# Kernel optimization log

Measured on AMD Instinct MI355X. Metric: run time of the kernel, lower is better.

Reference implementation:

```python
import jax, jax.numpy as jnp
import numpy as np

NUM_HEADS = 8
EMBED_CH = 512   # k channels
OUT_CH = 256     # v channels
MASK_CURRENT = False
NEG_INF = -1e30


def setup_inputs() -> dict:
    key = jax.random.key(0)
    ks = jax.random.split(key, 7)
    N, C, H, W = 8, 256, 32, 32
    s = lambda fan: 1.0 / np.sqrt(fan)
    return {
        "x": jax.random.normal(ks[0], (N, C, H, W), jnp.float32),
        "Wq": jax.random.normal(ks[1], (EMBED_CH, C), jnp.float32) * s(C),
        "bq": jax.random.normal(ks[2], (EMBED_CH,), jnp.float32) * 0.01,
        "Wkv": jax.random.normal(ks[3], (EMBED_CH + OUT_CH, C), jnp.float32) * s(C),
        "bkv": jax.random.normal(ks[4], (EMBED_CH + OUT_CH,), jnp.float32) * 0.01,
        "Wo": jax.random.normal(ks[5], (OUT_CH, OUT_CH), jnp.float32) * s(OUT_CH),
        "bo": jax.random.normal(ks[6], (OUT_CH,), jnp.float32) * 0.01,
    }


def _to_multihead(t, n, T):
    # t: [n, h*d, T] with channel layout '(h d)' -> [n, h, T, d]
    h = NUM_HEADS
    return t.reshape(n, h, -1, T).transpose(0, 1, 3, 2)


def reference(x, Wq, bq, Wkv, bkv, Wo, bo):
    n, C, H, W = x.shape
    T = H * W
    xf = x.reshape(n, C, T)  # flatten spatial dims into sequence

    # 1x1 convs == pointwise channel GEMMs
    q = jnp.einsum('oc,nct->not', Wq, xf) + bq[None, :, None]
    kv = jnp.einsum('oc,nct->not', Wkv, xf) + bkv[None, :, None]
    k, v = kv[:, :EMBED_CH], kv[:, EMBED_CH:]

    q = _to_multihead(q, n, T)   # [n, h, T, dk]
    k = _to_multihead(k, n, T)   # [n, h, T, dk]
    v = _to_multihead(v, n, T)   # [n, h, T, dv]

    dk = k.shape[-1]
    scale = 1.0 / np.sqrt(dk).astype(np.float32)

    # causal mask over flattened spatial positions (lower-triangular)
    diag = -1 if MASK_CURRENT else 0
    mask = jnp.tril(jnp.ones((T, T), dtype=bool), k=diag)  # [T, T]

    attn = jnp.einsum('nhtd,nhsd->nhts', q, k) * scale
    attn = jnp.where(mask[None, None], attn, NEG_INF)
    attn = jax.nn.softmax(attn, axis=-1)
    attn = jnp.where(mask[None, None], attn, 0.0)

    out = jnp.einsum('nhts,nhsd->nhtd', attn, v)            # [n, h, T, dv]
    out = out.transpose(0, 1, 3, 2).reshape(n, OUT_CH, T)   # n (h d) t

    out = jnp.einsum('oc,nct->not', Wo, out) + bo[None, :, None]
    return out.reshape(n, OUT_CH, H, W)
```

## Files before the change

### kernel.cpp

```cpp
#include <hip/hip_runtime.h>
#include <hip/hip_bf16.h>
#include <math.h>

typedef __bf16 bf16;
typedef __attribute__((ext_vector_type(4))) __bf16 bf16x4;
typedef __attribute__((ext_vector_type(8))) __bf16 bf16x8;
typedef __attribute__((ext_vector_type(4))) float f32x4;

#define T_DIM 1024
#define C_DIM 256
#define HEADS 8

static __device__ __forceinline__ int tb(int row, int col) {
  return row * 128 + ((((col >> 3) ^ row) & 7) << 4) + ((col & 7) << 1);
}

static __device__ __forceinline__ void gl16(const char* g, char* l) {
  __builtin_amdgcn_global_load_lds(
      (const __attribute__((address_space(1))) unsigned int*)g,
      (__attribute__((address_space(3))) unsigned int*)l, 16, 0, 0);
}
static __device__ __forceinline__ void stage16k(const char* g, char* l, int tid) {
  const int w = (tid >> 6) * 1024, ln = (tid & 63) * 16;
#pragma unroll
  for (int i = 0; i < 4; ++i) gl16(g + i * 4096 + w + ln, l + i * 4096 + w);
}
static __device__ __forceinline__ void stage8k(const char* g, char* l, int tid) {
  const int w = (tid >> 6) * 1024, ln = (tid & 63) * 16;
#pragma unroll
  for (int i = 0; i < 2; ++i) gl16(g + i * 4096 + w + ln, l + i * 4096 + w);
}
static __device__ __forceinline__ void stage4k(const char* g, char* l, int tid) {
  gl16(g + (tid >> 6) * 1024 + (tid & 63) * 16, l + (tid >> 6) * 1024);
}

__global__ __launch_bounds__(256) void k_prep(const float* __restrict__ x,
    const float* __restrict__ Wq, const float* __restrict__ Wkv, const float* __restrict__ Wo,
    char* __restrict__ xTt, char* __restrict__ Wbt, char* __restrict__ Wot) {
  const int tid = threadIdx.x;
  const int b = blockIdx.x;
  if (b < 512) {
    __shared__ float tile[64][65];
    const int n = b >> 6, rem = b & 63, tt64 = rem >> 2, ct = (rem & 3) << 6;
    const float* xp = x + ((size_t)n * C_DIM + ct) * T_DIM + tt64 * 64;
    const int t = tid & 63, c0 = tid >> 6;
#pragma unroll
    for (int i = 0; i < 16; ++i) tile[c0 + i * 4][t] = xp[(size_t)(c0 + i * 4) * T_DIM + t];
    __syncthreads();
    char* dst = xTt + (((size_t)(n * 8 + (tt64 >> 1))) * 4 + (rem & 3)) * 16384;
    const int rbase = (tt64 & 1) * 64;
#pragma unroll
    for (int i = 0; i < 2; ++i) {
      const int idx = tid + i * 256;
      const int tl = idx >> 3, c8 = (idx & 7) * 8;
      bf16x8 v;
#pragma unroll
      for (int j = 0; j < 8; ++j) v[j] = (bf16)tile[c8 + j][tl];
      *(bf16x8*)(dst + tb(rbase + tl, c8)) = v;
    }
  } else {
    const bool isWo = (b >= 532);
    const int o0 = (b - (isWo ? 532 : 512)) * 64;
#pragma unroll
    for (int i = 0; i < 8; ++i) {
      const int idx = tid + i * 256;
      const int row = idx >> 5, c8 = (idx & 31) * 8;
      const int o = o0 + row;
      const float* src = isWo ? (Wo + (size_t)o * C_DIM + c8)
                              : (o < 512 ? Wq + (size_t)o * C_DIM + c8
                                         : Wkv + (size_t)(o - 512) * C_DIM + c8);
      float4 a = *(const float4*)src;
      float4 bq4 = *(const float4*)(src + 4);
      bf16x8 v;
      v[0]=(bf16)a.x; v[1]=(bf16)a.y; v[2]=(bf16)a.z; v[3]=(bf16)a.w;
      v[4]=(bf16)bq4.x; v[5]=(bf16)bq4.y; v[6]=(bf16)bq4.z; v[7]=(bf16)bq4.w;
      char* base = isWo ? Wot : Wbt;
      char* dst = base + (((size_t)(o >> 7)) * 4 + (c8 >> 6)) * 16384;
      *(bf16x8*)(dst + tb(o & 127, c8 & 63)) = v;
    }
  }
}

__global__ __launch_bounds__(256) void k_qkv(const char* __restrict__ Wbt, const char* __restrict__ xTt,
    const float* __restrict__ bq, const float* __restrict__ bkv,
    bf16* __restrict__ q_ws, char* __restrict__ Kt, char* __restrict__ Vt) {
  __shared__ __attribute__((aligned(128))) unsigned char smem[32768];
  const int tid = threadIdx.x;
  const int nt = blockIdx.x, mt = blockIdx.y, n = blockIdx.z;
  const int w = tid >> 6, lane = tid & 63, lrow = lane & 15, lg = lane >> 4;
  const int wm = (w >> 1) * 64, wn = (w & 1) * 64;
  const char* gA = Wbt + (size_t)mt * 65536;
  const char* gB = xTt + ((size_t)(n * 8 + nt)) * 65536;

  f32x4 acc[4][4] = {};
#pragma unroll 1
  for (int kk = 0; kk < 4; ++kk) {
    stage16k(gA + kk * 16384, (char*)smem, tid);
    stage16k(gB + kk * 16384, (char*)smem + 16384, tid);
    __syncthreads();
    const char* As = (const char*)smem;
    const char* Bs = As + 16384;
    bf16x8 af[4][2], bv[4][2];
#pragma unroll
    for (int mi = 0; mi < 4; ++mi)
#pragma unroll
      for (int kh = 0; kh < 2; ++kh)
        af[mi][kh] = *(const bf16x8*)(As + tb(wm + mi * 16 + lrow, kh * 32 + lg * 8));
#pragma unroll
    for (int ni = 0; ni < 4; ++ni)
#pragma unroll
      for (int kh = 0; kh < 2; ++kh)
        bv[ni][kh] = *(const bf16x8*)(Bs + tb(wn + ni * 16 + lrow, kh * 32 + lg * 8));
#pragma unroll
    for (int kh = 0; kh < 2; ++kh)
#pragma unroll
      for (int mi = 0; mi < 4; ++mi)
#pragma unroll
        for (int ni = 0; ni < 4; ++ni)
          acc[mi][ni] = __builtin_amdgcn_mfma_f32_16x16x32_bf16(af[mi][kh], bv[ni][kh], acc[mi][ni], 0, 0, 0);
    __syncthreads();
  }

  const int obase = mt * 128 + wm + lg * 4;
  const int tcol0 = nt * 128 + wn + lrow;
#pragma unroll
  for (int mi = 0; mi < 4; ++mi) {
    const int o = obase + mi * 16;
    if (mt < 4) {
      const float4 bb = *(const float4*)(bq + o);
      const int nh = n * 8 + (o >> 6), d = o & 63;
      bf16* qrow = q_ws + (size_t)nh * (T_DIM * 64) + d;
#pragma unroll
      for (int ni = 0; ni < 4; ++ni) {
        const int t = tcol0 + ni * 16;
        f32x4 v = acc[mi][ni];
        bf16x4 pk;
        pk[0]=(bf16)(v[0]+bb.x); pk[1]=(bf16)(v[1]+bb.y); pk[2]=(bf16)(v[2]+bb.z); pk[3]=(bf16)(v[3]+bb.w);
        *(bf16x4*)(qrow + (size_t)t * 64) = pk;
      }
    } else if (mt < 8) {
      const int o2 = o - 512;
      const float4 bb = *(const float4*)(bkv + o2);
      const int nh = n * 8 + (o2 >> 6), d = o2 & 63;
      char* tbase = Kt + (size_t)nh * 16 * 8192;
#pragma unroll
      for (int ni = 0; ni < 4; ++ni) {
        const int t = tcol0 + ni * 16;
        f32x4 v = acc[mi][ni];
        bf16x4 pk;
        pk[0]=(bf16)(v[0]+bb.x); pk[1]=(bf16)(v[1]+bb.y); pk[2]=(bf16)(v[2]+bb.z); pk[3]=(bf16)(v[3]+bb.w);
        *(bf16x4*)(tbase + (t >> 6) * 8192 + tb(t & 63, d)) = pk;
      }
    } else {
      const int o3 = o - 1024;
      const float4 bb = *(const float4*)(bkv + 512 + o3);
      const float* bbp = (const float*)&bb;
      const int nh = n * 8 + (o3 >> 5), dv = o3 & 31;
      char* tbase = Vt + (size_t)nh * 16 * 4096;
#pragma unroll
      for (int ni = 0; ni < 4; ++ni) {
        const int t = tcol0 + ni * 16;
        f32x4 v = acc[mi][ni];
        char* tile = tbase + (t >> 6) * 4096;
#pragma unroll
        for (int r = 0; r < 4; ++r)
          *(bf16*)(tile + tb(dv + r, t & 63)) = (bf16)(v[r] + bbp[r]);
      }
    }
  }
}

__global__ __launch_bounds__(256) void k_attn(const bf16* __restrict__ q_ws,
    const char* __restrict__ Kt, const char* __restrict__ Vt, char* __restrict__ attTt) {
  __shared__ __attribute__((aligned(128))) unsigned char smem[20480];
  const int tid = threadIdx.x;
  const int nh = blockIdx.x, qp = blockIdx.y;
  const int w = tid >> 6, lane = tid & 63, lrow = lane & 15, lg = lane >> 4;

  const char* Ktb = Kt + (size_t)nh * 16 * 8192;
  const char* Vtb = Vt + (size_t)nh * 16 * 4096;
  const char* Kb = (const char*)smem;
  const char* Vb = (const char*)smem + 8192;
  char* pw = (char*)smem + 12288 + w * 2048;
  const int n = nh >> 3, h = nh & 7;
  const float s2 = 0.18033688f;

#pragma unroll 1
  for (int ph = 0; ph < 2; ++ph) {
    const int qt = ph ? (15 - qp) : qp;
    const int tg = qt * 64 + w * 16 + lrow;
    const bf16* qbase = q_ws + ((size_t)nh * T_DIM + tg) * 64;
    const bf16x8 qf0 = *(const bf16x8*)(qbase + lg * 8);
    const bf16x8 qf1 = *(const bf16x8*)(qbase + 32 + lg * 8);

    float m = -INFINITY, l = 0.f;
    f32x4 oacc[2] = {};

    for (int st = 0; st <= qt; ++st) {
      stage8k(Ktb + st * 8192, (char*)smem, tid);
      stage4k(Vtb + st * 4096, (char*)smem + 8192, tid);
      __syncthreads();

      f32x4 sacc[4];
#pragma unroll
      for (int rt = 0; rt < 4; ++rt) {
        f32x4 a = {0.f, 0.f, 0.f, 0.f};
        bf16x8 kf0 = *(const bf16x8*)(Kb + tb(rt * 16 + lrow, lg * 8));
        a = __builtin_amdgcn_mfma_f32_16x16x32_bf16(kf0, qf0, a, 0, 0, 0);
        bf16x8 kf1 = *(const bf16x8*)(Kb + tb(rt * 16 + lrow, 32 + lg * 8));
        a = __builtin_amdgcn_mfma_f32_16x16x32_bf16(kf1, qf1, a, 0, 0, 0);
        sacc[rt] = a;
      }

      float p[16];
      const bool diag = (st == qt);
      const int tl = w * 16 + lrow;
#pragma unroll
      for (int rt = 0; rt < 4; ++rt)
#pragma unroll
        for (int r = 0; r < 4; ++r) {
          float v = sacc[rt][r] * s2;
          if (diag && (rt * 16 + lg * 4 + r) > tl) v = -INFINITY;
          p[rt * 4 + r] = v;
        }

      float pmax = p[0];
#pragma unroll
      for (int i = 1; i < 16; ++i) pmax = fmaxf(pmax, p[i]);
      pmax = fmaxf(pmax, __shfl_xor(pmax, 16));
      pmax = fmaxf(pmax, __shfl_xor(pmax, 32));
      const float mn = fmaxf(m, pmax);
      const float corr = exp2f(m - mn);
      float ps = 0.f;
#pragma unroll
      for (int i = 0; i < 16; ++i) { p[i] = exp2f(p[i] - mn); ps += p[i]; }
      ps += __shfl_xor(ps, 16);
      ps += __shfl_xor(ps, 32);
      l = l * corr + ps;
      m = mn;
      oacc[0] = oacc[0] * corr;
      oacc[1] = oacc[1] * corr;

#pragma unroll
      for (int rt = 0; rt < 4; ++rt) {
        bf16x4 pk;
#pragma unroll
        for (int r = 0; r < 4; ++r) pk[r] = (bf16)p[rt * 4 + r];
        *(bf16x4*)(pw + tb(lrow, rt * 16 + lg * 4)) = pk;
      }

#pragma unroll
      for (int ks = 0; ks < 2; ++ks) {
        bf16x8 pf = *(const bf16x8*)(pw + tb(lrow, ks * 32 + lg * 8));
#pragma unroll
        for (int dt = 0; dt < 2; ++dt) {
          bf16x8 vf = *(const bf16x8*)(Vb + tb(dt * 16 + lrow, ks * 32 + lg * 8));
          oacc[dt] = __builtin_amdgcn_mfma_f32_16x16x32_bf16(vf, pf, oacc[dt], 0, 0, 0);
        }
      }
      __syncthreads();
    }

    const float inv = 1.0f / l;
    const int ntt = tg >> 7, row = tg & 127;
#pragma unroll
    for (int dt = 0; dt < 2; ++dt) {
      const int c = h * 32 + dt * 16 + lg * 4;
      char* tile = attTt + (((size_t)(n * 8 + ntt)) * 4 + (c >> 6)) * 16384;
      bf16x4 pk;
#pragma unroll
      for (int r = 0; r < 4; ++r) pk[r] = (bf16)(oacc[dt][r] * inv);
      *(bf16x4*)(tile + tb(row, c & 63)) = pk;
    }
  }
}

__global__ __launch_bounds__(256) void k_proj(const char* __restrict__ attTt,
    const char* __restrict__ Wot, const float* __restrict__ bo, float* __restrict__ out) {
  __shared__ __attribute__((aligned(128))) unsigned char smem[24576];
  const int tid = threadIdx.x;
  const int tm = blockIdx.x, om = blockIdx.y, n = blockIdx.z;
  const int w = tid >> 6, lane = tid & 63, lrow = lane & 15, lg = lane >> 4;
  const int wm = (w >> 1) * 64, wn = (w & 1) * 32;
  const char* gA = attTt + ((size_t)(n * 8 + tm)) * 65536;
  const char* gB = Wot + (size_t)(om >> 1) * 65536 + (om & 1) * 8192;

  f32x4 acc[4][2] = {};
#pragma unroll 1
  for (int kk = 0; kk < 4; ++kk) {
    stage16k(gA + kk * 16384, (char*)smem, tid);
    stage8k(gB + kk * 16384, (char*)smem + 16384, tid);
    __syncthreads();
    const char* As = (const char*)smem;
    const char* Bs = As + 16384;
    bf16x8 af[4][2], bv[2][2];
#pragma unroll
    for (int mi = 0; mi < 4; ++mi)
#pragma unroll
      for (int kh = 0; kh < 2; ++kh)
        af[mi][kh] = *(const bf16x8*)(As + tb(wm + mi * 16 + lrow, kh * 32 + lg * 8));
#pragma unroll
    for (int ni = 0; ni < 2; ++ni)
#pragma unroll
      for (int kh = 0; kh < 2; ++kh)
        bv[ni][kh] = *(const bf16x8*)(Bs + tb(wn + ni * 16 + lrow, kh * 32 + lg * 8));
#pragma unroll
    for (int kh = 0; kh < 2; ++kh)
#pragma unroll
      for (int mi = 0; mi < 4; ++mi)
#pragma unroll
        for (int ni = 0; ni < 2; ++ni)
          acc[mi][ni] = __builtin_amdgcn_mfma_f32_16x16x32_bf16(af[mi][kh], bv[ni][kh], acc[mi][ni], 0, 0, 0);
    __syncthreads();
  }

  const int t0b = tm * 128 + wm + lg * 4;
  const int ob = om * 64 + wn + lrow;
#pragma unroll
  for (int mi = 0; mi < 4; ++mi) {
    const int t0 = t0b + mi * 16;
#pragma unroll
    for (int ni = 0; ni < 2; ++ni) {
      const int o = ob + ni * 16;
      const float bb = bo[o];
      f32x4 v = acc[mi][ni];
      v[0] += bb; v[1] += bb; v[2] += bb; v[3] += bb;
      *(f32x4*)(out + ((size_t)(n * C_DIM + o)) * T_DIM + t0) = v;
    }
  }
}

extern "C" void kernel_launch(void* const* d_in, const int* in_sizes, int n_in,
                              void* d_out, int out_size, void* d_ws, size_t ws_size,
                              hipStream_t stream) {
  const float* x   = (const float*)d_in[0];
  const float* Wq  = (const float*)d_in[1];
  const float* bq  = (const float*)d_in[2];
  const float* Wkv = (const float*)d_in[3];
  const float* bkv = (const float*)d_in[4];
  const float* Wo  = (const float*)d_in[5];
  const float* bo  = (const float*)d_in[6];
  float* out = (float*)d_out;

  char* ws = (char*)d_ws;
  char* xTt   = ws;
  char* Wbt   = ws + (4u  << 20);
  char* Wot   = ws + (5u  << 20);
  bf16* q_ws  = (bf16*)(ws + (6u << 20));
  char* Kt    = ws + (14u << 20);
  char* Vt    = ws + (22u << 20);
  char* attTt = ws + (26u << 20);

  k_prep<<<536, 256, 0, stream>>>(x, Wq, Wkv, Wo, xTt, Wbt, Wot);
  k_qkv<<<dim3(8, 10, 8), 256, 0, stream>>>(Wbt, xTt, bq, bkv, q_ws, Kt, Vt);
  k_attn<<<dim3(64, 8), 256, 0, stream>>>(q_ws, Kt, Vt, attTt);
  k_proj<<<dim3(8, 4, 8), 256, 0, stream>>>(attTt, Wot, bo, out);
}
```

Baseline: 60.59 us.

## Share K/V tiles across paired query tiles, stage V via LDS, vectorize prep

The attention kernel now handles both paired query tiles (qp and 15-qp) in one pass over the key/value tiles. It stages two K/V tiles per barrier and reuses each staged tile for both query tiles, which halves global K/V loads and barriers, and it adds s_setprio around the MFMA sections. The QKV kernel writes V through a padded LDS transpose so the global stores are vectorized 16-byte writes instead of scattered 2-byte ones. The x transpose in prep uses float4 loads, and the output projection uses smaller 64-row tiles to double the grid. In exchange the attention kernel doubles its LDS use and keeps two sets of accumulators live.

```diff
diff --git a/kernel.cpp b/kernel.cpp
--- a/kernel.cpp
+++ b/kernel.cpp
@@ -43,9 +43,13 @@
     __shared__ float tile[64][65];
     const int n = b >> 6, rem = b & 63, tt64 = rem >> 2, ct = (rem & 3) << 6;
     const float* xp = x + ((size_t)n * C_DIM + ct) * T_DIM + tt64 * 64;
-    const int t = tid & 63, c0 = tid >> 6;
-#pragma unroll
-    for (int i = 0; i < 16; ++i) tile[c0 + i * 4][t] = xp[(size_t)(c0 + i * 4) * T_DIM + t];
+    const int t4 = (tid & 15) * 4, c0 = tid >> 4;
+#pragma unroll
+    for (int i = 0; i < 4; ++i) {
+      const int c = c0 + i * 16;
+      float4 v = *(const float4*)(xp + (size_t)c * T_DIM + t4);
+      tile[c][t4] = v.x; tile[c][t4 + 1] = v.y; tile[c][t4 + 2] = v.z; tile[c][t4 + 3] = v.w;
+    }
     __syncthreads();
     char* dst = xTt + (((size_t)(n * 8 + (tt64 >> 1))) * 4 + (rem & 3)) * 16384;
     const int rbase = (tt64 & 1) * 64;
@@ -84,7 +88,7 @@
 __global__ __launch_bounds__(256) void k_qkv(const char* __restrict__ Wbt, const char* __restrict__ xTt,
     const float* __restrict__ bq, const float* __restrict__ bkv,
     bf16* __restrict__ q_ws, char* __restrict__ Kt, char* __restrict__ Vt) {
-  __shared__ __attribute__((aligned(128))) unsigned char smem[32768];
+  __shared__ __attribute__((aligned(128))) unsigned char smem[34816];
   const int tid = threadIdx.x;
   const int nt = blockIdx.x, mt = blockIdx.y, n = blockIdx.z;
   const int w = tid >> 6, lane = tid & 63, lrow = lane & 15, lg = lane >> 4;
@@ -123,179 +127,215 @@
 
   const int obase = mt * 128 + wm + lg * 4;
   const int tcol0 = nt * 128 + wn + lrow;
-#pragma unroll
-  for (int mi = 0; mi < 4; ++mi) {
-    const int o = obase + mi * 16;
-    if (mt < 4) {
-      const float4 bb = *(const float4*)(bq + o);
-      const int nh = n * 8 + (o >> 6), d = o & 63;
-      bf16* qrow = q_ws + (size_t)nh * (T_DIM * 64) + d;
+  if (mt < 8) {
+#pragma unroll
+    for (int mi = 0; mi < 4; ++mi) {
+      const int o = obase + mi * 16;
+      if (mt < 4) {
+        const float4 bb = *(const float4*)(bq + o);
+        const int nh = n * 8 + (o >> 6), d = o & 63;
+        bf16* qrow = q_ws + (size_t)nh * (T_DIM * 64) + d;
+#pragma unroll
+        for (int ni = 0; ni < 4; ++ni) {
+          const int t = tcol0 + ni * 16;
+          f32x4 v = acc[mi][ni];
+          bf16x4 pk;
+          pk[0]=(bf16)(v[0]+bb.x); pk[1]=(bf16)(v[1]+bb.y); pk[2]=(bf16)(v[2]+bb.z); pk[3]=(bf16)(v[3]+bb.w);
+          *(bf16x4*)(qrow + (size_t)t * 64) = pk;
+        }
+      } else {
+        const int o2 = o - 512;
+        const float4 bb = *(const float4*)(bkv + o2);
+        const int nh = n * 8 + (o2 >> 6), d = o2 & 63;
+        char* tbase = Kt + (size_t)nh * 16 * 8192;
+#pragma unroll
+        for (int ni = 0; ni < 4; ++ni) {
+          const int t = tcol0 + ni * 16;
+          f32x4 v = acc[mi][ni];
+          bf16x4 pk;
+          pk[0]=(bf16)(v[0]+bb.x); pk[1]=(bf16)(v[1]+bb.y); pk[2]=(bf16)(v[2]+bb.z); pk[3]=(bf16)(v[3]+bb.w);
+          *(bf16x4*)(tbase + (t >> 6) * 8192 + tb(t & 63, d)) = pk;
+        }
+      }
+    }
+  } else {
+    bf16* tp = (bf16*)smem;
+#pragma unroll
+    for (int mi = 0; mi < 4; ++mi) {
+      const int o3g = (mt - 8) * 128 + wm + mi * 16 + lg * 4;
+      const float4 bb = *(const float4*)(bkv + 512 + o3g);
+      const float* bbp = (const float*)&bb;
+      const int o3l = wm + mi * 16 + lg * 4;
 #pragma unroll
       for (int ni = 0; ni < 4; ++ni) {
-        const int t = tcol0 + ni * 16;
+        const int tl = wn + ni * 16 + lrow;
         f32x4 v = acc[mi][ni];
-        bf16x4 pk;
-        pk[0]=(bf16)(v[0]+bb.x); pk[1]=(bf16)(v[1]+bb.y); pk[2]=(bf16)(v[2]+bb.z); pk[3]=(bf16)(v[3]+bb.w);
-        *(bf16x4*)(qrow + (size_t)t * 64) = pk;
+#pragma unroll
+        for (int r = 0; r < 4; ++r)
+          tp[(o3l + r) * 132 + tl] = (bf16)(v[r] + bbp[r]);
       }
-    } else if (mt < 8) {
-      const int o2 = o - 512;
-      const float4 bb = *(const float4*)(bkv + o2);
-      const int nh = n * 8 + (o2 >> 6), d = o2 & 63;
-      char* tbase = Kt + (size_t)nh * 16 * 8192;
-#pragma unroll
-      for (int ni = 0; ni < 4; ++ni) {
-        const int t = tcol0 + ni * 16;
-        f32x4 v = acc[mi][ni];
-        bf16x4 pk;
-        pk[0]=(bf16)(v[0]+bb.x); pk[1]=(bf16)(v[1]+bb.y); pk[2]=(bf16)(v[2]+bb.z); pk[3]=(bf16)(v[3]+bb.w);
-        *(bf16x4*)(tbase + (t >> 6) * 8192 + tb(t & 63, d)) = pk;
-      }
-    } else {
-      const int o3 = o - 1024;
-      const float4 bb = *(const float4*)(bkv + 512 + o3);
-      const float* bbp = (const float*)&bb;
-      const int nh = n * 8 + (o3 >> 5), dv = o3 & 31;
-      char* tbase = Vt + (size_t)nh * 16 * 4096;
-#pragma unroll
-      for (int ni = 0; ni < 4; ++ni) {
-        const int t = tcol0 + ni * 16;
-        f32x4 v = acc[mi][ni];
-        char* tile = tbase + (t >> 6) * 4096;
-#pragma unroll
-        for (int r = 0; r < 4; ++r)
-          *(bf16*)(tile + tb(dv + r, t & 63)) = (bf16)(v[r] + bbp[r]);
-      }
+    }
+    __syncthreads();
+    const int row = tid >> 1, half = tid & 1;
+    const int o3 = (mt - 8) * 128 + row;
+    const int nh = n * 8 + (o3 >> 5), dv = o3 & 31;
+    char* tile = Vt + (size_t)nh * 16 * 4096 + (nt * 2 + half) * 4096;
+    const bf16* src = tp + row * 132 + half * 64;
+#pragma unroll
+    for (int g = 0; g < 8; ++g) {
+      bf16x4 lo = *(const bf16x4*)(src + g * 8);
+      bf16x4 hi = *(const bf16x4*)(src + g * 8 + 4);
+      bf16x8 vv;
+      vv[0]=lo[0]; vv[1]=lo[1]; vv[2]=lo[2]; vv[3]=lo[3];
+      vv[4]=hi[0]; vv[5]=hi[1]; vv[6]=hi[2]; vv[7]=hi[3];
+      *(bf16x8*)(tile + tb(dv, g * 8)) = vv;
     }
   }
 }
 
 __global__ __launch_bounds__(256) void k_attn(const bf16* __restrict__ q_ws,
     const char* __restrict__ Kt, const char* __restrict__ Vt, char* __restrict__ attTt) {
-  __shared__ __attribute__((aligned(128))) unsigned char smem[20480];
+  __shared__ __attribute__((aligned(128))) unsigned char smem[40960];
   const int tid = threadIdx.x;
   const int nh = blockIdx.x, qp = blockIdx.y;
   const int w = tid >> 6, lane = tid & 63, lrow = lane & 15, lg = lane >> 4;
-
+  const int tl = w * 16 + lrow;
   const char* Ktb = Kt + (size_t)nh * 16 * 8192;
   const char* Vtb = Vt + (size_t)nh * 16 * 4096;
-  const char* Kb = (const char*)smem;
-  const char* Vb = (const char*)smem + 8192;
-  char* pw = (char*)smem + 12288 + w * 2048;
   const int n = nh >> 3, h = nh & 7;
   const float s2 = 0.18033688f;
 
+  const int qt0 = qp, qt1 = 15 - qp;
+  const int tg0 = qt0 * 64 + tl, tg1 = qt1 * 64 + tl;
+  const bf16* qb0 = q_ws + ((size_t)nh * T_DIM + tg0) * 64;
+  const bf16* qb1 = q_ws + ((size_t)nh * T_DIM + tg1) * 64;
+  const bf16x8 qA0 = *(const bf16x8*)(qb0 + lg * 8);
+  const bf16x8 qA1 = *(const bf16x8*)(qb0 + 32 + lg * 8);
+  const bf16x8 qB0 = *(const bf16x8*)(qb1 + lg * 8);
+  const bf16x8 qB1 = *(const bf16x8*)(qb1 + 32 + lg * 8);
+
+  float m0 = -INFINITY, l0 = 0.f, m1 = -INFINITY, l1 = 0.f;
+  f32x4 o0a = {}, o0b = {}, o1a = {}, o1b = {};
+
+  auto proc = [&](bf16x8 qf0, bf16x8 qf1, float& m, float& l, f32x4& oa, f32x4& ob,
+                  const char* Kbs, const char* Vbs, char* pws, bool diag) {
+    f32x4 sacc[4];
+    __builtin_amdgcn_s_setprio(1);
+#pragma unroll
+    for (int rt = 0; rt < 4; ++rt) {
+      f32x4 a = {0.f, 0.f, 0.f, 0.f};
+      bf16x8 kf0 = *(const bf16x8*)(Kbs + tb(rt * 16 + lrow, lg * 8));
+      a = __builtin_amdgcn_mfma_f32_16x16x32_bf16(kf0, qf0, a, 0, 0, 0);
+      bf16x8 kf1 = *(const bf16x8*)(Kbs + tb(rt * 16 + lrow, 32 + lg * 8));
+      a = __builtin_amdgcn_mfma_f32_16x16x32_bf16(kf1, qf1, a, 0, 0, 0);
+      sacc[rt] = a;
+    }
+    __builtin_amdgcn_s_setprio(0);
+    float p[16];
+#pragma unroll
+    for (int rt = 0; rt < 4; ++rt)
+#pragma unroll
+      for (int r = 0; r < 4; ++r) {
+        float v = sacc[rt][r] * s2;
+        if (diag && (rt * 16 + lg * 4 + r) > tl) v = -INFINITY;
+        p[rt * 4 + r] = v;
+      }
+    float pmax = p[0];
+#pragma unroll
+    for (int i = 1; i < 16; ++i) pmax = fmaxf(pmax, p[i]);
+    pmax = fmaxf(pmax, __shfl_xor(pmax, 16));
+    pmax = fmaxf(pmax, __shfl_xor(pmax, 32));
+    const float mn = fmaxf(m, pmax);
+    const float corr = exp2f(m - mn);
+    float ps = 0.f;
+#pragma unroll
+    for (int i = 0; i < 16; ++i) { p[i] = exp2f(p[i] - mn); ps += p[i]; }
+    ps += __shfl_xor(ps, 16);
+    ps += __shfl_xor(ps, 32);
+    l = l * corr + ps;
+    m = mn;
+    oa = oa * corr;
+    ob = ob * corr;
+#pragma unroll
+    for (int rt = 0; rt < 4; ++rt) {
+      bf16x4 pk;
+#pragma unroll
+      for (int r = 0; r < 4; ++r) pk[r] = (bf16)p[rt * 4 + r];
+      *(bf16x4*)(pws + tb(lrow, rt * 16 + lg * 4)) = pk;
+    }
+    __builtin_amdgcn_s_setprio(1);
+#pragma unroll
+    for (int ks = 0; ks < 2; ++ks) {
+      bf16x8 pf = *(const bf16x8*)(pws + tb(lrow, ks * 32 + lg * 8));
+      bf16x8 vf0 = *(const bf16x8*)(Vbs + tb(lrow, ks * 32 + lg * 8));
+      oa = __builtin_amdgcn_mfma_f32_16x16x32_bf16(vf0, pf, oa, 0, 0, 0);
+      bf16x8 vf1 = *(const bf16x8*)(Vbs + tb(16 + lrow, ks * 32 + lg * 8));
+      ob = __builtin_amdgcn_mfma_f32_16x16x32_bf16(vf1, pf, ob, 0, 0, 0);
+    }
+    __builtin_amdgcn_s_setprio(0);
+  };
+
 #pragma unroll 1
-  for (int ph = 0; ph < 2; ++ph) {
-    const int qt = ph ? (15 - qp) : qp;
-    const int tg = qt * 64 + w * 16 + lrow;
-    const bf16* qbase = q_ws + ((size_t)nh * T_DIM + tg) * 64;
-    const bf16x8 qf0 = *(const bf16x8*)(qbase + lg * 8);
-    const bf16x8 qf1 = *(const bf16x8*)(qbase + 32 + lg * 8);
-
-    float m = -INFINITY, l = 0.f;
-    f32x4 oacc[2] = {};
-
-    for (int st = 0; st <= qt; ++st) {
-      stage8k(Ktb + st * 8192, (char*)smem, tid);
-      stage4k(Vtb + st * 4096, (char*)smem + 8192, tid);
-      __syncthreads();
-
-      f32x4 sacc[4];
-#pragma unroll
-      for (int rt = 0; rt < 4; ++rt) {
-        f32x4 a = {0.f, 0.f, 0.f, 0.f};
-        bf16x8 kf0 = *(const bf16x8*)(Kb + tb(rt * 16 + lrow, lg * 8));
-        a = __builtin_amdgcn_mfma_f32_16x16x32_bf16(kf0, qf0, a, 0, 0, 0);
-        bf16x8 kf1 = *(const bf16x8*)(Kb + tb(rt * 16 + lrow, 32 + lg * 8));
-        a = __builtin_amdgcn_mfma_f32_16x16x32_bf16(kf1, qf1, a, 0, 0, 0);
-        sacc[rt] = a;
-      }
-
-      float p[16];
-      const bool diag = (st == qt);
-      const int tl = w * 16 + lrow;
-#pragma unroll
-      for (int rt = 0; rt < 4; ++rt)
-#pragma unroll
-        for (int r = 0; r < 4; ++r) {
-          float v = sacc[rt][r] * s2;
-          if (diag && (rt * 16 + lg * 4 + r) > tl) v = -INFINITY;
-          p[rt * 4 + r] = v;
-        }
-
-      float pmax = p[0];
-#pragma unroll
-      for (int i = 1; i < 16; ++i) pmax = fmaxf(pmax, p[i]);
-      pmax = fmaxf(pmax, __shfl_xor(pmax, 16));
-      pmax = fmaxf(pmax, __shfl_xor(pmax, 32));
-      const float mn = fmaxf(m, pmax);
-      const float corr = exp2f(m - mn);
-      float ps = 0.f;
-#pragma unroll
-      for (int i = 0; i < 16; ++i) { p[i] = exp2f(p[i] - mn); ps += p[i]; }
-      ps += __shfl_xor(ps, 16);
-      ps += __shfl_xor(ps, 32);
-      l = l * corr + ps;
-      m = mn;
-      oacc[0] = oacc[0] * corr;
-      oacc[1] = oacc[1] * corr;
-
-#pragma unroll
-      for (int rt = 0; rt < 4; ++rt) {
-        bf16x4 pk;
-#pragma unroll
-        for (int r = 0; r < 4; ++r) pk[r] = (bf16)p[rt * 4 + r];
-        *(bf16x4*)(pw + tb(lrow, rt * 16 + lg * 4)) = pk;
-      }
-
-#pragma unroll
-      for (int ks = 0; ks < 2; ++ks) {
-        bf16x8 pf = *(const bf16x8*)(pw + tb(lrow, ks * 32 + lg * 8));
-#pragma unroll
-        for (int dt = 0; dt < 2; ++dt) {
-          bf16x8 vf = *(const bf16x8*)(Vb + tb(dt * 16 + lrow, ks * 32 + lg * 8));
-          oacc[dt] = __builtin_amdgcn_mfma_f32_16x16x32_bf16(vf, pf, oacc[dt], 0, 0, 0);
-        }
-      }
-      __syncthreads();
-    }
-
+  for (int st2 = 0; st2 <= qt1; st2 += 2) {
+    const bool has1 = (st2 + 1 <= qt1);
+    stage8k(Ktb + (size_t)st2 * 8192, (char*)smem, tid);
+    if (has1) stage8k(Ktb + (size_t)(st2 + 1) * 8192, (char*)smem + 8192, tid);
+    stage4k(Vtb + (size_t)st2 * 4096, (char*)smem + 16384, tid);
+    if (has1) stage4k(Vtb + (size_t)(st2 + 1) * 4096, (char*)smem + 20480, tid);
+    __syncthreads();
+    const int nsub = has1 ? 2 : 1;
+#pragma unroll 1
+    for (int sub = 0; sub < nsub; ++sub) {
+      const int stk = st2 + sub;
+      const char* Kbs = (const char*)smem + sub * 8192;
+      const char* Vbs = (const char*)smem + 16384 + sub * 4096;
+      char* pws = (char*)smem + 24576 + w * 4096 + sub * 2048;
+      proc(qB0, qB1, m1, l1, o1a, o1b, Kbs, Vbs, pws, stk == qt1);
+      if (stk <= qt0)
+        proc(qA0, qA1, m0, l0, o0a, o0b, Kbs, Vbs, pws, stk == qt0);
+    }
+    __syncthreads();
+  }
+
+  auto epi = [&](int tg, float l, f32x4 oa, f32x4 ob) {
     const float inv = 1.0f / l;
     const int ntt = tg >> 7, row = tg & 127;
 #pragma unroll
     for (int dt = 0; dt < 2; ++dt) {
+      const f32x4 v = dt ? ob : oa;
       const int c = h * 32 + dt * 16 + lg * 4;
       char* tile = attTt + (((size_t)(n * 8 + ntt)) * 4 + (c >> 6)) * 16384;
       bf16x4 pk;
 #pragma unroll
-      for (int r = 0; r < 4; ++r) pk[r] = (bf16)(oacc[dt][r] * inv);
+      for (int r = 0; r < 4; ++r) pk[r] = (bf16)(v[r] * inv);
       *(bf16x4*)(tile + tb(row, c & 63)) = pk;
     }
-  }
+  };
+  epi(tg0, l0, o0a, o0b);
+  epi(tg1, l1, o1a, o1b);
 }
 
 __global__ __launch_bounds__(256) void k_proj(const char* __restrict__ attTt,
     const char* __restrict__ Wot, const float* __restrict__ bo, float* __restrict__ out) {
-  __shared__ __attribute__((aligned(128))) unsigned char smem[24576];
+  __shared__ __attribute__((aligned(128))) unsigned char smem[16384];
   const int tid = threadIdx.x;
   const int tm = blockIdx.x, om = blockIdx.y, n = blockIdx.z;
   const int w = tid >> 6, lane = tid & 63, lrow = lane & 15, lg = lane >> 4;
-  const int wm = (w >> 1) * 64, wn = (w & 1) * 32;
-  const char* gA = attTt + ((size_t)(n * 8 + tm)) * 65536;
+  const int wm = (w >> 1) * 32, wn = (w & 1) * 32;
+  const char* gA = attTt + ((size_t)(n * 8 + (tm >> 1))) * 65536 + (tm & 1) * 8192;
   const char* gB = Wot + (size_t)(om >> 1) * 65536 + (om & 1) * 8192;
 
-  f32x4 acc[4][2] = {};
+  f32x4 acc[2][2] = {};
 #pragma unroll 1
   for (int kk = 0; kk < 4; ++kk) {
-    stage16k(gA + kk * 16384, (char*)smem, tid);
-    stage8k(gB + kk * 16384, (char*)smem + 16384, tid);
+    stage8k(gA + kk * 16384, (char*)smem, tid);
+    stage8k(gB + kk * 16384, (char*)smem + 8192, tid);
     __syncthreads();
     const char* As = (const char*)smem;
-    const char* Bs = As + 16384;
-    bf16x8 af[4][2], bv[2][2];
-#pragma unroll
-    for (int mi = 0; mi < 4; ++mi)
+    const char* Bs = As + 8192;
+    bf16x8 af[2][2], bv[2][2];
+#pragma unroll
+    for (int mi = 0; mi < 2; ++mi)
 #pragma unroll
       for (int kh = 0; kh < 2; ++kh)
         af[mi][kh] = *(const bf16x8*)(As + tb(wm + mi * 16 + lrow, kh * 32 + lg * 8));
@@ -307,17 +347,17 @@
 #pragma unroll
     for (int kh = 0; kh < 2; ++kh)
 #pragma unroll
-      for (int mi = 0; mi < 4; ++mi)
+      for (int mi = 0; mi < 2; ++mi)
 #pragma unroll
         for (int ni = 0; ni < 2; ++ni)
           acc[mi][ni] = __builtin_amdgcn_mfma_f32_16x16x32_bf16(af[mi][kh], bv[ni][kh], acc[mi][ni], 0, 0, 0);
     __syncthreads();
   }
 
-  const int t0b = tm * 128 + wm + lg * 4;
+  const int t0b = tm * 64 + wm + lg * 4;
   const int ob = om * 64 + wn + lrow;
 #pragma unroll
-  for (int mi = 0; mi < 4; ++mi) {
+  for (int mi = 0; mi < 2; ++mi) {
     const int t0 = t0b + mi * 16;
 #pragma unroll
     for (int ni = 0; ni < 2; ++ni) {
@@ -354,5 +394,5 @@
   k_prep<<<536, 256, 0, stream>>>(x, Wq, Wkv, Wo, xTt, Wbt, Wot);
   k_qkv<<<dim3(8, 10, 8), 256, 0, stream>>>(Wbt, xTt, bq, bkv, q_ws, Kt, Vt);
   k_attn<<<dim3(64, 8), 256, 0, stream>>>(q_ws, Kt, Vt, attTt);
-  k_proj<<<dim3(8, 4, 8), 256, 0, stream>>>(attTt, Wot, bo, out);
-}
+  k_proj<<<dim3(16, 4, 8), 256, 0, stream>>>(attTt, Wot, bo, out);
+}
```

New measurement: 59.58 us. No clear change (-1.7%).
